# Kernel optimization log

Hardware: AMD Instinct MI355X
Metric: run time of the kernel (lower is better)

The kernel has to match this reference:

```python
import jax, jax.numpy as jnp
from jax import lax
import numpy as np

RADIUS = 0.1
NSAMPLE = 32
STRIDE = 4
NUM_DIR = 32
BN_EPS = 1e-5


def _fps(p, m):
    # furthest point sampling: p (B,N,3) -> (B,m) int32 indices, start at index 0
    B, N, _ = p.shape

    def step(carry, _):
        dists, last = carry
        lp = jnp.take_along_axis(p, jnp.broadcast_to(last[:, None, None], (B, 1, 3)), axis=1)
        d = jnp.sum((p - lp) ** 2, axis=-1)
        dists = jnp.minimum(dists, d)
        nxt = jnp.argmax(dists, axis=-1).astype(jnp.int32)
        return (dists, nxt), nxt

    last0 = jnp.zeros((B,), jnp.int32)
    d0 = jnp.full((B, N), 1e10, p.dtype)
    _, rest = lax.scan(step, (d0, last0), None, length=m - 1)
    return jnp.concatenate([last0[None, :], rest], axis=0).T  # (B, m)


def _ball_query(q, p, k, radius):
    # q (B,M,3) centers, p (B,N,3) support -> (B,M,k) indices of first k points in ball,
    # padded with the first found index (PointNet++ convention)
    N = p.shape[1]
    d2 = jnp.sum((q[:, :, None, :] - p[:, None, :, :]) ** 2, axis=-1)  # (B,M,N)
    cand = jnp.where(d2 < radius * radius, jnp.arange(N, dtype=jnp.int32), N)
    cand = jnp.sort(cand, axis=-1)[:, :, :k]
    first = cand[:, :, :1]
    return jnp.where(cand == N, first, cand)


def _bn(x, g, b, m, v):
    # BatchNorm1d eval mode on (B,C,N)
    return (x - m[:, None]) * (g[:, None] / jnp.sqrt(v[:, None] + BN_EPS)) + b[:, None]


def _normalize(x, axis):
    return x / jnp.maximum(jnp.linalg.norm(x, axis=axis, keepdims=True), 1e-12)


def setup_inputs() -> dict:
    key = jax.random.key(0)
    ks = jax.random.split(key, 16)
    B, N, Cin, Cout = 4, 8192, 128, 256
    half = Cout // 2
    s = 0.02
    return {
        "p": jax.random.uniform(ks[0], (B, N, 3), jnp.float32),
        "f": jax.random.normal(ks[1], (B, Cin, N), jnp.float32),
        "conv1_w": jax.random.normal(ks[2], (Cout, Cin), jnp.float32) * s,
        "conv1_b": jax.random.normal(ks[3], (Cout,), jnp.float32) * s,
        "skip_w": jax.random.normal(ks[4], (Cout, Cin), jnp.float32) * s,
        "skip_b": jax.random.normal(ks[5], (Cout,), jnp.float32) * s,
        "bn1_g": jnp.ones((Cout,), jnp.float32),
        "bn1_b": jnp.zeros((Cout,), jnp.float32),
        "bn1_m": jax.random.normal(ks[6], (Cout,), jnp.float32) * 0.1,
        "bn1_v": jax.random.uniform(ks[7], (Cout,), jnp.float32) + 0.5,
        "dir_vectors": jax.random.normal(ks[8], (NUM_DIR, 3), jnp.float32),
        "de_w1": jax.random.normal(ks[9], (half, NUM_DIR), jnp.float32) * s,
        "de_g": jnp.ones((half,), jnp.float32),
        "de_bb": jnp.zeros((half,), jnp.float32),
        "de_m": jax.random.normal(ks[10], (half,), jnp.float32) * 0.1,
        "de_v": jax.random.uniform(ks[11], (half,), jnp.float32) + 0.5,
        "de_w2": jax.random.normal(ks[12], (Cout, half), jnp.float32) * s,
        "de_b2": jax.random.normal(ks[13], (Cout,), jnp.float32) * s,
    }


def reference(p, f, conv1_w, conv1_b, skip_w, skip_b, bn1_g, bn1_b, bn1_m, bn1_v,
              dir_vectors, de_w1, de_g, de_bb, de_m, de_v, de_w2, de_b2):
    B, N, _ = p.shape
    Cout = conv1_w.shape[0]
    M, K = N // STRIDE, NSAMPLE

    # FPS sampling + centroid gather
    idx = _fps(p, M)  # (B,M)
    new_p = jnp.take_along_axis(p, jnp.broadcast_to(idx[:, :, None], (B, M, 3)), axis=1)

    # residual branch: gather input feats at centroids, 1x1 conv (bn_after=False)
    fi = jnp.take_along_axis(f, jnp.broadcast_to(idx[:, None, :], (B, f.shape[1], M)), axis=2)
    identity = jnp.einsum('oc,bcm->bom', skip_w, fi) + skip_b[:, None]

    # convs1: 1x1 conv on all N points
    f1 = jnp.einsum('oc,bcn->bon', conv1_w, f) + conv1_b[:, None]  # (B,Cout,N)

    # ball-query grouping
    qidx = _ball_query(new_p, p, K, RADIUS)  # (B,M,K)
    idxf = qidx.reshape(B, M * K)
    gp = jnp.take_along_axis(p, jnp.broadcast_to(idxf[:, :, None], (B, M * K, 3)), axis=1).reshape(B, M, K, 3)
    dp = jnp.transpose(gp - new_p[:, :, None, :], (0, 3, 1, 2))  # (B,3,M,K)
    fj = jnp.take_along_axis(f1, jnp.broadcast_to(idxf[:, None, :], (B, Cout, M * K)), axis=2).reshape(B, Cout, M, K)

    # directional encoding
    dpn = _normalize(dp, axis=1)
    vec = _normalize(dir_vectors, axis=1)  # (NUM_DIR,3)
    theta = jnp.einsum('md,bdnk->bmnk', vec, dpn)  # (B,NUM_DIR,M,K)
    tmax = theta.max(axis=-1)  # (B,NUM_DIR,M)
    h = jnp.einsum('om,bmn->bon', de_w1, tmax)
    h = jax.nn.gelu(_bn(h, de_g, de_bb, de_m, de_v), approximate=False)
    pe = jnp.einsum('oc,bcn->bon', de_w2, h) + de_b2[:, None]

    # neighbor max-pool + BN + residuals
    f_out = _bn(fj.max(axis=-1), bn1_g, bn1_b, bn1_m, bn1_v) + pe + identity
    return new_p, f_out
```

## Files before the change

kernel.cpp:

```cpp
#include <hip/hip_runtime.h>

#define BATCH 4
#define NPTS 8192
#define MPTS 2048
#define CIN 128
#define CO 256
#define KS 32
#define ND 32
#define HALF 128

typedef unsigned int u32;
typedef unsigned long long u64;

#define DPPC_QUAD_XOR1 0xB1
#define DPPC_QUAD_XOR2 0x4E
#define DPPC_ROW_MIRROR 0x140
#define DPPC_ROW_HALF_MIRROR 0x141
#define DPPC_ROW_BCAST15 0x142
#define DPPC_ROW_BCAST31 0x143

template<int CTRL>
__device__ __forceinline__ float dpp_max(float v) {
    int o = __builtin_amdgcn_update_dpp(__float_as_int(-1e30f), __float_as_int(v),
                                        CTRL, 0xF, 0xF, false);
    return fmaxf(v, __int_as_float(o));
}
__device__ __forceinline__ float wave_max_f32(float v) {
    v = dpp_max<DPPC_QUAD_XOR1>(v);
    v = dpp_max<DPPC_QUAD_XOR2>(v);
    v = dpp_max<DPPC_ROW_HALF_MIRROR>(v);
    v = dpp_max<DPPC_ROW_MIRROR>(v);
    v = dpp_max<DPPC_ROW_BCAST15>(v);
    v = dpp_max<DPPC_ROW_BCAST31>(v);
    return __int_as_float(__builtin_amdgcn_readlane(__float_as_int(v), 63));
}

__global__ __launch_bounds__(512, 2) void k_fps_f1(
    const float* __restrict__ p, const float* __restrict__ f,
    const float* __restrict__ conv1_w, const float* __restrict__ conv1_b,
    float* __restrict__ out_newp, int* __restrict__ idx,
    float* __restrict__ f1t) {
    __shared__ __align__(16) char smem_u[33024];
    if (blockIdx.x < 4) {
        u64*   wkey = (u64*)smem_u;
        int*   sidx = (int*)(smem_u + 128);
        float* sx   = (float*)(smem_u + 128 + 4 * MPTS);
        float* sy   = sx + MPTS;
        float* sz   = sy + MPTS;
        int b = blockIdx.x, t = threadIdx.x;
        int lane = t & 63, wid = t >> 6;
        int j0 = t * 16;
        const float* pb = p + (size_t)b * NPTS * 3;
        const float* pt = pb + t * 48;
        float px[16], py[16], pz[16], dist[16];
#pragma unroll
        for (int c = 0; c < 4; ++c) {
            float4 q0 = *(const float4*)(pt + c * 12 + 0);
            float4 q1 = *(const float4*)(pt + c * 12 + 4);
            float4 q2 = *(const float4*)(pt + c * 12 + 8);
            px[c*4+0] = q0.x; py[c*4+0] = q0.y; pz[c*4+0] = q0.z;
            px[c*4+1] = q0.w; py[c*4+1] = q1.x; pz[c*4+1] = q1.y;
            px[c*4+2] = q1.z; py[c*4+2] = q1.w; pz[c*4+2] = q2.x;
            px[c*4+3] = q2.y; py[c*4+3] = q2.z; pz[c*4+3] = q2.w;
        }
#pragma unroll
        for (int i = 0; i < 16; ++i) dist[i] = 1e10f;
        float lx = pb[0], ly = pb[1], lz = pb[2];
        if (t == 0) {
            sidx[0] = 0; sx[0] = lx; sy[0] = ly; sz[0] = lz;
        }
        for (int s = 1; s < MPTS; ++s) {
            int par = s & 1;
            float bv = -1e30f; int bi = 0;
#pragma unroll
            for (int i = 0; i < 16; ++i) {
                float dx = __fsub_rn(px[i], lx);
                float dy = __fsub_rn(py[i], ly);
                float dz = __fsub_rn(pz[i], lz);
                float d  = __fadd_rn(__fadd_rn(__fmul_rn(dx, dx), __fmul_rn(dy, dy)),
                                     __fmul_rn(dz, dz));
                float nd = fminf(dist[i], d);
                dist[i] = nd;
                bool gt = nd > bv;
                bi = gt ? i : bi;
                bv = fmaxf(bv, nd);
            }
            float gmw = wave_max_f32(bv);
            u64 mask = __ballot(bv == gmw);
            int first = __ffsll((long long)mask) - 1;
            if (lane == first) {
                wkey[par * 8 + wid] = ((u64)__float_as_uint(gmw) << 32)
                                    | (u64)(u32)(NPTS - 1 - (j0 + bi));
            }
            __syncthreads();
            const u64* wk = wkey + par * 8;
            u64 k0 = wk[0], k1 = wk[1], k2 = wk[2], k3 = wk[3];
            u64 k4 = wk[4], k5 = wk[5], k6 = wk[6], k7 = wk[7];
            u64 m01 = k1 > k0 ? k1 : k0;
            u64 m23 = k3 > k2 ? k3 : k2;
            u64 m45 = k5 > k4 ? k5 : k4;
            u64 m67 = k7 > k6 ? k7 : k6;
            u64 m03 = m23 > m01 ? m23 : m01;
            u64 m47 = m67 > m45 ? m67 : m45;
            u64 best = m47 > m03 ? m47 : m03;
            int w0 = (NPTS - 1 - (int)(best & 0xFFFFFFFFull)) & (NPTS - 1);
            int w0s = __builtin_amdgcn_readfirstlane(w0);
            lx = pb[w0s * 3 + 0]; ly = pb[w0s * 3 + 1]; lz = pb[w0s * 3 + 2];
            if (t == 0) {
                sidx[s] = w0s; sx[s] = lx; sy[s] = ly; sz[s] = lz;
            }
        }
        __syncthreads();
        for (int e = t; e < MPTS; e += 512) {
            int base = (b * MPTS + e) * 3;
            out_newp[base + 0] = sx[e];
            out_newp[base + 1] = sy[e];
            out_newp[base + 2] = sz[e];
            idx[b * MPTS + e] = sidx[e];
        }
    } else if (f1t != nullptr) {
        float* fT = (float*)smem_u;
        int blk = blockIdx.x - 4;
        int b = blk >> 8;
        int n0 = (blk & 255) << 5;
        int t = threadIdx.x;
        const float* fb = f + (size_t)b * CIN * NPTS;
        for (int e = t; e < CIN * 32; e += 512) {
            int k = e >> 5, j = e & 31;
            fT[e] = fb[(size_t)k * NPTS + n0 + j];
        }
        __syncthreads();
        int c = t & 255, jh = (t >> 8) << 4;
        float bias = conv1_b[c];
        float acc[16];
#pragma unroll
        for (int j = 0; j < 16; ++j) acc[j] = bias;
        const float4* wrow4 = (const float4*)(conv1_w + (size_t)c * CIN);
        const float4* fT4 = (const float4*)fT;
        for (int k4 = 0; k4 < 32; ++k4) {
            float4 wv = wrow4[k4];
#pragma unroll
            for (int sub = 0; sub < 4; ++sub) {
                float w = sub == 0 ? wv.x : sub == 1 ? wv.y : sub == 2 ? wv.z : wv.w;
                int k = k4 * 4 + sub;
                int base = (k * 32 + jh) >> 2;
                float4 a0 = fT4[base+0], a1 = fT4[base+1], a2 = fT4[base+2], a3 = fT4[base+3];
                acc[0]  = fmaf(w, a0.x, acc[0]);  acc[1]  = fmaf(w, a0.y, acc[1]);
                acc[2]  = fmaf(w, a0.z, acc[2]);  acc[3]  = fmaf(w, a0.w, acc[3]);
                acc[4]  = fmaf(w, a1.x, acc[4]);  acc[5]  = fmaf(w, a1.y, acc[5]);
                acc[6]  = fmaf(w, a1.z, acc[6]);  acc[7]  = fmaf(w, a1.w, acc[7]);
                acc[8]  = fmaf(w, a2.x, acc[8]);  acc[9]  = fmaf(w, a2.y, acc[9]);
                acc[10] = fmaf(w, a2.z, acc[10]); acc[11] = fmaf(w, a2.w, acc[11]);
                acc[12] = fmaf(w, a3.x, acc[12]); acc[13] = fmaf(w, a3.y, acc[13]);
                acc[14] = fmaf(w, a3.z, acc[14]); acc[15] = fmaf(w, a3.w, acc[15]);
            }
        }
        float* dst = f1t + ((size_t)b * NPTS + n0 + jh) * CO + c;
#pragma unroll
        for (int j = 0; j < 16; ++j) dst[(size_t)j * CO] = acc[j];
    }
}

__global__ __launch_bounds__(256) void k_f1(const float* __restrict__ f,
                                            const float* __restrict__ conv1_w,
                                            const float* __restrict__ conv1_b,
                                            float* __restrict__ f1t, int b0) {
    __shared__ __align__(16) float fT[CIN * 16];
    int blk = blockIdx.x;
    int bl = blk >> 9;
    int b = b0 + bl;
    int n0 = (blk & 511) << 4;
    int t = threadIdx.x;
    const float* fb = f + (size_t)b * CIN * NPTS;
    for (int e = t; e < CIN * 16; e += 256) {
        int k = e >> 4, j = e & 15;
        fT[e] = fb[(size_t)k * NPTS + n0 + j];
    }
    __syncthreads();
    int c = t;
    float bias = conv1_b[c];
    float acc[16];
#pragma unroll
    for (int j = 0; j < 16; ++j) acc[j] = bias;
    const float4* wrow4 = (const float4*)(conv1_w + (size_t)c * CIN);
    const float4* fT4 = (const float4*)fT;
    for (int k4 = 0; k4 < 32; ++k4) {
        float4 wv = wrow4[k4];
#pragma unroll
        for (int sub = 0; sub < 4; ++sub) {
            float w = sub == 0 ? wv.x : sub == 1 ? wv.y : sub == 2 ? wv.z : wv.w;
            int k = k4 * 4 + sub;
            float4 a0 = fT4[k*4+0], a1 = fT4[k*4+1], a2 = fT4[k*4+2], a3 = fT4[k*4+3];
            acc[0]  = fmaf(w, a0.x, acc[0]);  acc[1]  = fmaf(w, a0.y, acc[1]);
            acc[2]  = fmaf(w, a0.z, acc[2]);  acc[3]  = fmaf(w, a0.w, acc[3]);
            acc[4]  = fmaf(w, a1.x, acc[4]);  acc[5]  = fmaf(w, a1.y, acc[5]);
            acc[6]  = fmaf(w, a1.z, acc[6]);  acc[7]  = fmaf(w, a1.w, acc[7]);
            acc[8]  = fmaf(w, a2.x, acc[8]);  acc[9]  = fmaf(w, a2.y, acc[9]);
            acc[10] = fmaf(w, a2.z, acc[10]); acc[11] = fmaf(w, a2.w, acc[11]);
            acc[12] = fmaf(w, a3.x, acc[12]); acc[13] = fmaf(w, a3.y, acc[13]);
            acc[14] = fmaf(w, a3.z, acc[14]); acc[15] = fmaf(w, a3.w, acc[15]);
        }
    }
    float* dst = f1t + ((size_t)bl * NPTS + n0) * CO + c;
#pragma unroll
    for (int j = 0; j < 16; ++j) dst[(size_t)j * CO] = acc[j];
}

__global__ __launch_bounds__(256) void k_feat(
    const float* __restrict__ p, const float* __restrict__ f,
    const float* __restrict__ f1t,
    const float* __restrict__ skip_w,  const float* __restrict__ skip_b,
    const float* __restrict__ bn1_g, const float* __restrict__ bn1_b,
    const float* __restrict__ bn1_m, const float* __restrict__ bn1_v,
    const float* __restrict__ dirv,  const float* __restrict__ de_w1,
    const float* __restrict__ de_g,  const float* __restrict__ de_bb,
    const float* __restrict__ de_m,  const float* __restrict__ de_v,
    const float* __restrict__ de_w2, const float* __restrict__ de_b2,
    const int* __restrict__ idx,     float* __restrict__ out_f, int b0) {
    __shared__ float sdx[KS], sdy[KS], sdz[KS];
    __shared__ float ltm[ND], lfi[CIN], lh[HALF];
    __shared__ int swidx[4][KS];
    __shared__ int scnt[4];
    __shared__ int nb[KS], nbp[KS];

    int q = b0 * MPTS + blockIdx.x;
    int b = q >> 11;
    int bl = b - b0;
    int m = q & (MPTS - 1);
    int t = threadIdx.x, lane = t & 63, w = t >> 6;
    const float* pb = p + (size_t)b * NPTS * 3;
    int i0 = idx[q] & (NPTS - 1);
    float qx = pb[i0 * 3 + 0], qy = pb[i0 * 3 + 1], qz = pb[i0 * 3 + 2];
    const float R2 = 0.1f * 0.1f;

    int cnt = 0;
    int seg = w * 2048;
    for (int base = 0; base < 2048; base += 64) {
        int j = seg + base + lane;
        float dx = __fsub_rn(pb[j * 3 + 0], qx);
        float dy = __fsub_rn(pb[j * 3 + 1], qy);
        float dz = __fsub_rn(pb[j * 3 + 2], qz);
        float d2 = __fadd_rn(__fadd_rn(__fmul_rn(dx, dx), __fmul_rn(dy, dy)),
                             __fmul_rn(dz, dz));
        bool hit = d2 < R2;
        u64 mask = __ballot(hit);
        if (hit) {
            int pos = cnt + __popcll(mask & ((1ull << lane) - 1ull));
            if (pos < KS) swidx[w][pos] = j;
        }
        cnt += __popcll(mask);
        if (cnt >= KS) break;
    }
    if (lane == 0) scnt[w] = cnt < KS ? cnt : KS;
    __syncthreads();
    int c0s = scnt[0], c1s = scnt[1], c2s = scnt[2], c3s = scnt[3];
    int st1 = c0s, st2 = c0s + c1s, st3 = c0s + c1s + c2s;
    int total = c0s + c1s + c2s + c3s; if (total > KS) total = KS;
    if (total < 1) total = 1;
    if (t < 128) {
        int ww = t >> 5, l = t & 31;
        int stw = (ww == 0) ? 0 : (ww == 1) ? st1 : (ww == 2) ? st2 : st3;
        int cw  = (ww == 0) ? c0s : (ww == 1) ? c1s : (ww == 2) ? c2s : c3s;
        int gp = stw + l;
        if (l < cw && gp < KS) nb[gp] = swidx[ww][l];
    }
    __syncthreads();
    if (t < KS) {
        int jk = nb[t < total ? t : 0] & (NPTS - 1);
        nbp[t] = jk;
        float dx = pb[jk * 3 + 0] - qx;
        float dy = pb[jk * 3 + 1] - qy;
        float dz = pb[jk * 3 + 2] - qz;
        float nr = fmaxf(sqrtf(dx * dx + dy * dy + dz * dz), 1e-12f);
        sdx[t] = dx / nr; sdy[t] = dy / nr; sdz[t] = dz / nr;
    }
    if (t >= 128) {
        lfi[t - 128] = f[((size_t)b * CIN + (t - 128)) * NPTS + i0];
    }
    __syncthreads();
    if (t < ND) {
        float ax = dirv[t * 3], ay = dirv[t * 3 + 1], az = dirv[t * 3 + 2];
        float n = fmaxf(sqrtf(ax * ax + ay * ay + az * az), 1e-12f);
        float vx = ax / n, vy = ay / n, vz = az / n;
        float tm = -1e30f;
#pragma unroll
        for (int k = 0; k < KS; ++k)
            tm = fmaxf(tm, vx * sdx[k] + vy * sdy[k] + vz * sdz[k]);
        ltm[t] = tm;
    }
    __syncthreads();

    int c = t;
    const float* f1b = f1t + (size_t)bl * NPTS * CO + c;
    float mx = -1e30f;
#pragma unroll 8
    for (int k = 0; k < KS; ++k) {
        mx = fmaxf(mx, f1b[(size_t)nbp[k] * CO]);
    }
    float sc1 = bn1_g[c] / sqrtf(bn1_v[c] + 1e-5f);
    float o1 = (mx - bn1_m[c]) * sc1 + bn1_b[c];

    float idv = skip_b[c];
    {
        const float4* sr = (const float4*)(skip_w + (size_t)c * CIN);
#pragma unroll 8
        for (int r = 0; r < 32; ++r) {
            float4 v = sr[r];
            idv = fmaf(v.x, lfi[r*4+0], fmaf(v.y, lfi[r*4+1],
                  fmaf(v.z, lfi[r*4+2], fmaf(v.w, lfi[r*4+3], idv))));
        }
    }
    {
        int hc = c & (HALF - 1);
        const float4* d1 = (const float4*)(de_w1 + (size_t)hc * ND);
        float a = 0.0f;
#pragma unroll
        for (int r = 0; r < 8; ++r) {
            float4 v = d1[r];
            a = fmaf(v.x, ltm[r*4+0], fmaf(v.y, ltm[r*4+1],
                fmaf(v.z, ltm[r*4+2], fmaf(v.w, ltm[r*4+3], a))));
        }
        float dsc = de_g[hc] / sqrtf(de_v[hc] + 1e-5f);
        float xb = (a - de_m[hc]) * dsc + de_bb[hc];
        float hv = 0.5f * xb * (1.0f + erff(xb * 0.70710678118654752440f));
        if (c < HALF) lh[c] = hv;
    }
    __syncthreads();
    float pe = de_b2[c];
    {
        const float4* d2p = (const float4*)(de_w2 + (size_t)c * HALF);
#pragma unroll 8
        for (int r = 0; r < 32; ++r) {
            float4 v = d2p[r];
            pe = fmaf(v.x, lh[r*4+0], fmaf(v.y, lh[r*4+1],
                 fmaf(v.z, lh[r*4+2], fmaf(v.w, lh[r*4+3], pe))));
        }
    }
    out_f[((size_t)b * CO + c) * MPTS + m] = o1 + pe + idv;
}

__global__ __launch_bounds__(256) void k_featz_fused(
    const float* __restrict__ p, const float* __restrict__ f,
    const float* __restrict__ conv1_w, const float* __restrict__ conv1_b,
    const float* __restrict__ skip_w,  const float* __restrict__ skip_b,
    const float* __restrict__ bn1_g, const float* __restrict__ bn1_b,
    const float* __restrict__ bn1_m, const float* __restrict__ bn1_v,
    const float* __restrict__ dirv,  const float* __restrict__ de_w1,
    const float* __restrict__ de_g,  const float* __restrict__ de_bb,
    const float* __restrict__ de_m,  const float* __restrict__ de_v,
    const float* __restrict__ de_w2, const float* __restrict__ de_b2,
    const int* __restrict__ idx,     float* __restrict__ out_f) {
    __shared__ __align__(16) float fg[KS * CIN];
    __shared__ float sdx[KS], sdy[KS], sdz[KS];
    __shared__ float ltm[ND], lfi[CIN], lh[HALF];
    __shared__ int swidx[4][KS];
    __shared__ int scnt[4];
    __shared__ int nb[KS], nbp[KS];

    int q = blockIdx.x;
    int b = q >> 11;
    int m = q & (MPTS - 1);
    int t = threadIdx.x, lane = t & 63, w = t >> 6;
    const float* pb = p + (size_t)b * NPTS * 3;
    int i0 = idx[q] & (NPTS - 1);
    float qx = pb[i0 * 3 + 0], qy = pb[i0 * 3 + 1], qz = pb[i0 * 3 + 2];
    const float R2 = 0.1f * 0.1f;
    int cnt = 0;
    int seg = w * 2048;
    for (int base = 0; base < 2048; base += 64) {
        int j = seg + base + lane;
        float dx = __fsub_rn(pb[j * 3 + 0], qx);
        float dy = __fsub_rn(pb[j * 3 + 1], qy);
        float dz = __fsub_rn(pb[j * 3 + 2], qz);
        float d2 = __fadd_rn(__fadd_rn(__fmul_rn(dx, dx), __fmul_rn(dy, dy)),
                             __fmul_rn(dz, dz));
        bool hit = d2 < R2;
        u64 mask = __ballot(hit);
        if (hit) {
            int pos = cnt + __popcll(mask & ((1ull << lane) - 1ull));
            if (pos < KS) swidx[w][pos] = j;
        }
        cnt += __popcll(mask);
        if (cnt >= KS) break;
    }
    if (lane == 0) scnt[w] = cnt < KS ? cnt : KS;
    __syncthreads();
    int c0s = scnt[0], c1s = scnt[1], c2s = scnt[2], c3s = scnt[3];
    int st1 = c0s, st2 = c0s + c1s, st3 = c0s + c1s + c2s;
    int total = c0s + c1s + c2s + c3s; if (total > KS) total = KS;
    if (total < 1) total = 1;
    if (t < 128) {
        int ww = t >> 5, l = t & 31;
        int stw = (ww == 0) ? 0 : (ww == 1) ? st1 : (ww == 2) ? st2 : st3;
        int cw  = (ww == 0) ? c0s : (ww == 1) ? c1s : (ww == 2) ? c2s : c3s;
        int gp = stw + l;
        if (l < cw && gp < KS) nb[gp] = swidx[ww][l];
    }
    __syncthreads();
    if (t < KS) {
        int jk = nb[t < total ? t : 0] & (NPTS - 1);
        nbp[t] = jk;
        float dx = pb[jk * 3 + 0] - qx;
        float dy = pb[jk * 3 + 1] - qy;
        float dz = pb[jk * 3 + 2] - qz;
        float nr = fmaxf(sqrtf(dx * dx + dy * dy + dz * dz), 1e-12f);
        sdx[t] = dx / nr; sdy[t] = dy / nr; sdz[t] = dz / nr;
    }
    if (t >= 128) lfi[t - 128] = f[((size_t)b * CIN + (t - 128)) * NPTS + i0];
    __syncthreads();
    if (t < ND) {
        float ax = dirv[t * 3], ay = dirv[t * 3 + 1], az = dirv[t * 3 + 2];
        float n = fmaxf(sqrtf(ax * ax + ay * ay + az * az), 1e-12f);
        float vx = ax / n, vy = ay / n, vz = az / n;
        float tm = -1e30f;
#pragma unroll
        for (int k = 0; k < KS; ++k)
            tm = fmaxf(tm, vx * sdx[k] + vy * sdy[k] + vz * sdz[k]);
        ltm[t] = tm;
    }
    for (int e = t; e < KS * CIN; e += 256) {
        int k = e >> 7, i = e & 127;
        fg[k * CIN + i] = f[((size_t)b * CIN + i) * NPTS + nbp[k]];
    }
    __syncthreads();
    int c = t;
    float acc[KS];
#pragma unroll
    for (int k = 0; k < KS; ++k) acc[k] = 0.0f;
    const float4* w4 = (const float4*)(conv1_w + (size_t)c * CIN);
    const float4* fg4 = (const float4*)fg;
    for (int i4 = 0; i4 < 32; ++i4) {
        float4 wv = w4[i4];
#pragma unroll 8
        for (int k = 0; k < KS; ++k) {
            float4 g = fg4[k * 32 + i4];
            acc[k] = fmaf(wv.x, g.x, fmaf(wv.y, g.y,
                     fmaf(wv.z, g.z, fmaf(wv.w, g.w, acc[k]))));
        }
    }
    float bias = conv1_b[c];
    float mx = -1e30f;
#pragma unroll
    for (int k = 0; k < KS; ++k) mx = fmaxf(mx, acc[k] + bias);
    float sc1 = bn1_g[c] / sqrtf(bn1_v[c] + 1e-5f);
    float o1 = (mx - bn1_m[c]) * sc1 + bn1_b[c];
    float idv = skip_b[c];
    {
        const float4* sr = (const float4*)(skip_w + (size_t)c * CIN);
#pragma unroll 8
        for (int r = 0; r < 32; ++r) {
            float4 v = sr[r];
            idv = fmaf(v.x, lfi[r*4+0], fmaf(v.y, lfi[r*4+1],
                  fmaf(v.z, lfi[r*4+2], fmaf(v.w, lfi[r*4+3], idv))));
        }
    }
    {
        int hc = c & (HALF - 1);
        const float4* d1 = (const float4*)(de_w1 + (size_t)hc * ND);
        float a = 0.0f;
#pragma unroll
        for (int r = 0; r < 8; ++r) {
            float4 v = d1[r];
            a = fmaf(v.x, ltm[r*4+0], fmaf(v.y, ltm[r*4+1],
                fmaf(v.z, ltm[r*4+2], fmaf(v.w, ltm[r*4+3], a))));
        }
        float dsc = de_g[hc] / sqrtf(de_v[hc] + 1e-5f);
        float xb = (a - de_m[hc]) * dsc + de_bb[hc];
        float hv = 0.5f * xb * (1.0f + erff(xb * 0.70710678118654752440f));
        if (c < HALF) lh[c] = hv;
    }
    __syncthreads();
    float pe = de_b2[c];
    {
        const float4* d2p = (const float4*)(de_w2 + (size_t)c * HALF);
#pragma unroll 8
        for (int r = 0; r < 32; ++r) {
            float4 v = d2p[r];
            pe = fmaf(v.x, lh[r*4+0], fmaf(v.y, lh[r*4+1],
                 fmaf(v.z, lh[r*4+2], fmaf(v.w, lh[r*4+3], pe))));
        }
    }
    out_f[((size_t)b * CO + c) * MPTS + m] = o1 + pe + idv;
}

extern "C" void kernel_launch(void* const* d_in, const int* in_sizes, int n_in,
                              void* d_out, int out_size, void* d_ws, size_t ws_size,
                              hipStream_t stream) {
    const float* p       = (const float*)d_in[0];
    const float* f       = (const float*)d_in[1];
    const float* conv1_w = (const float*)d_in[2];
    const float* conv1_b = (const float*)d_in[3];
    const float* skip_w  = (const float*)d_in[4];
    const float* skip_b  = (const float*)d_in[5];
    const float* bn1_g   = (const float*)d_in[6];
    const float* bn1_b   = (const float*)d_in[7];
    const float* bn1_m   = (const float*)d_in[8];
    const float* bn1_v   = (const float*)d_in[9];
    const float* dirv    = (const float*)d_in[10];
    const float* de_w1   = (const float*)d_in[11];
    const float* de_g    = (const float*)d_in[12];
    const float* de_bb   = (const float*)d_in[13];
    const float* de_m    = (const float*)d_in[14];
    const float* de_v    = (const float*)d_in[15];
    const float* de_w2   = (const float*)d_in[16];
    const float* de_b2   = (const float*)d_in[17];

    float* out_newp = (float*)d_out;
    float* out_f    = (float*)d_out + (size_t)BATCH * MPTS * 3;
    int*   idx      = (int*)d_ws;
    float* f1t      = (float*)((char*)d_ws + 32768);

    size_t f1_one  = (size_t)NPTS * CO * 4;
    size_t need_full = 32768 + 4 * f1_one;
    size_t need_one  = 32768 + f1_one;
    int mode = (ws_size >= need_full) ? 2 : (ws_size >= need_one) ? 1 : 0;

    if (mode == 2) {
        k_fps_f1<<<dim3(4 + 1024), dim3(512), 0, stream>>>(
            p, f, conv1_w, conv1_b, out_newp, idx, f1t);
        k_feat<<<dim3(4 * MPTS), dim3(256), 0, stream>>>(
            p, f, f1t, skip_w, skip_b, bn1_g, bn1_b, bn1_m, bn1_v,
            dirv, de_w1, de_g, de_bb, de_m, de_v, de_w2, de_b2, idx, out_f, 0);
    } else if (mode == 1) {
        k_fps_f1<<<dim3(4), dim3(512), 0, stream>>>(
            p, f, conv1_w, conv1_b, out_newp, idx, nullptr);
        for (int b0 = 0; b0 < BATCH; ++b0) {
            k_f1  <<<dim3(512),  dim3(256), 0, stream>>>(f, conv1_w, conv1_b, f1t, b0);
            k_feat<<<dim3(MPTS), dim3(256), 0, stream>>>(
                p, f, f1t, skip_w, skip_b, bn1_g, bn1_b, bn1_m, bn1_v,
                dirv, de_w1, de_g, de_bb, de_m, de_v, de_w2, de_b2, idx, out_f, b0);
        }
    } else {
        k_fps_f1<<<dim3(4), dim3(512), 0, stream>>>(
            p, f, conv1_w, conv1_b, out_newp, idx, nullptr);
        k_featz_fused<<<dim3(BATCH * MPTS), dim3(256), 0, stream>>>(
            p, f, conv1_w, conv1_b, skip_w, skip_b, bn1_g, bn1_b, bn1_m, bn1_v,
            dirv, de_w1, de_g, de_bb, de_m, de_v, de_w2, de_b2, idx, out_f);
    }
}
```

Measured before the change: 2.857 ms.

## Fuse FPS, conv1 and feature stages into one persistent kernel with progress flags

Adds a single mega-kernel in which the four FPS blocks publish per-step progress counters through agent-scope atomics. Feature blocks spin-wait on those counters and on a conv1 completion counter, then do ball query, directional encoding and output for each sampled centre as soon as it exists. This overlaps the long serial FPS with the per-centre feature work and removes a kernel boundary. The cost is polling traffic, a memset, and the risk of deadlock or stale reads if blocks are not co-resident or ordering is weak, although the spin loops have iteration caps.

```diff
diff --git a/kernel.cpp b/kernel.cpp
--- a/kernel.cpp
+++ b/kernel.cpp
@@ -33,6 +33,299 @@
     v = dpp_max<DPPC_ROW_BCAST15>(v);
     v = dpp_max<DPPC_ROW_BCAST31>(v);
     return __int_as_float(__builtin_amdgcn_readlane(__float_as_int(v), 63));
+}
+
+struct FeatSmem {
+    float sdx[KS], sdy[KS], sdz[KS];
+    float ltm[ND], lfi[CIN], lh[HALF];
+    int swidx[4][KS];
+    int scnt[4];
+    int nb[KS], nbp[KS];
+};
+
+__global__ __launch_bounds__(512, 2) void k_mega(
+    const float* __restrict__ p, const float* __restrict__ f,
+    const float* __restrict__ conv1_w, const float* __restrict__ conv1_b,
+    const float* __restrict__ skip_w,  const float* __restrict__ skip_b,
+    const float* __restrict__ bn1_g, const float* __restrict__ bn1_b,
+    const float* __restrict__ bn1_m, const float* __restrict__ bn1_v,
+    const float* __restrict__ dirv,  const float* __restrict__ de_w1,
+    const float* __restrict__ de_g,  const float* __restrict__ de_bb,
+    const float* __restrict__ de_m,  const float* __restrict__ de_v,
+    const float* __restrict__ de_w2, const float* __restrict__ de_b2,
+    float* __restrict__ out_newp, float* __restrict__ out_f,
+    int* __restrict__ idx, float* __restrict__ f1t,
+    int* prog, int* f1all) {
+    __shared__ __align__(16) char smem_u[16640];
+    if (blockIdx.x < 4) {
+        u64* wkey = (u64*)smem_u;
+        int b = blockIdx.x, t = threadIdx.x;
+        int lane = t & 63, wid = t >> 6;
+        int j0 = t * 16;
+        const float* pb = p + (size_t)b * NPTS * 3;
+        const float* pt = pb + t * 48;
+        float px[16], py[16], pz[16], dist[16];
+#pragma unroll
+        for (int c = 0; c < 4; ++c) {
+            float4 q0 = *(const float4*)(pt + c * 12 + 0);
+            float4 q1 = *(const float4*)(pt + c * 12 + 4);
+            float4 q2 = *(const float4*)(pt + c * 12 + 8);
+            px[c*4+0] = q0.x; py[c*4+0] = q0.y; pz[c*4+0] = q0.z;
+            px[c*4+1] = q0.w; py[c*4+1] = q1.x; pz[c*4+1] = q1.y;
+            px[c*4+2] = q1.z; py[c*4+2] = q1.w; pz[c*4+2] = q2.x;
+            px[c*4+3] = q2.y; py[c*4+3] = q2.z; pz[c*4+3] = q2.w;
+        }
+#pragma unroll
+        for (int i = 0; i < 16; ++i) dist[i] = 1e10f;
+        float lx = pb[0], ly = pb[1], lz = pb[2];
+        if (t == 0) {
+            out_newp[(size_t)b * MPTS * 3 + 0] = lx;
+            out_newp[(size_t)b * MPTS * 3 + 1] = ly;
+            out_newp[(size_t)b * MPTS * 3 + 2] = lz;
+            __hip_atomic_store(idx + b * MPTS, 0, __ATOMIC_RELAXED,
+                               __HIP_MEMORY_SCOPE_AGENT);
+        }
+        for (int s = 1; s < MPTS; ++s) {
+            int par = s & 1;
+            float bv = -1e30f; int bi = 0;
+#pragma unroll
+            for (int i = 0; i < 16; ++i) {
+                float dx = __fsub_rn(px[i], lx);
+                float dy = __fsub_rn(py[i], ly);
+                float dz = __fsub_rn(pz[i], lz);
+                float d  = __fadd_rn(__fadd_rn(__fmul_rn(dx, dx), __fmul_rn(dy, dy)),
+                                     __fmul_rn(dz, dz));
+                float nd = fminf(dist[i], d);
+                dist[i] = nd;
+                bool gt = nd > bv;
+                bi = gt ? i : bi;
+                bv = fmaxf(bv, nd);
+            }
+            float gmw = wave_max_f32(bv);
+            u64 mask = __ballot(bv == gmw);
+            int first = __ffsll((long long)mask) - 1;
+            if (lane == first) {
+                wkey[par * 8 + wid] = ((u64)__float_as_uint(gmw) << 32)
+                                    | (u64)(u32)(NPTS - 1 - (j0 + bi));
+            }
+            __syncthreads();
+            const u64* wk = wkey + par * 8;
+            u64 k0 = wk[0], k1 = wk[1], k2 = wk[2], k3 = wk[3];
+            u64 k4 = wk[4], k5 = wk[5], k6 = wk[6], k7 = wk[7];
+            u64 m01 = k1 > k0 ? k1 : k0;
+            u64 m23 = k3 > k2 ? k3 : k2;
+            u64 m45 = k5 > k4 ? k5 : k4;
+            u64 m67 = k7 > k6 ? k7 : k6;
+            u64 m03 = m23 > m01 ? m23 : m01;
+            u64 m47 = m67 > m45 ? m67 : m45;
+            u64 best = m47 > m03 ? m47 : m03;
+            int w0 = (NPTS - 1 - (int)(best & 0xFFFFFFFFull)) & (NPTS - 1);
+            int w0s = __builtin_amdgcn_readfirstlane(w0);
+            if (t == 0) {
+                asm volatile("s_waitcnt vmcnt(0)" ::: "memory");
+                __hip_atomic_store(prog + b, s, __ATOMIC_RELAXED,
+                                   __HIP_MEMORY_SCOPE_AGENT);
+            }
+            lx = pb[w0s * 3 + 0]; ly = pb[w0s * 3 + 1]; lz = pb[w0s * 3 + 2];
+            if (t == 0) {
+                out_newp[((size_t)b * MPTS + s) * 3 + 0] = lx;
+                out_newp[((size_t)b * MPTS + s) * 3 + 1] = ly;
+                out_newp[((size_t)b * MPTS + s) * 3 + 2] = lz;
+                __hip_atomic_store(idx + b * MPTS + s, w0s, __ATOMIC_RELAXED,
+                                   __HIP_MEMORY_SCOPE_AGENT);
+            }
+        }
+        if (t == 0) {
+            asm volatile("s_waitcnt vmcnt(0)" ::: "memory");
+            __hip_atomic_store(prog + b, MPTS, __ATOMIC_RELAXED,
+                               __HIP_MEMORY_SCOPE_AGENT);
+        }
+    } else if (blockIdx.x < 4 + 1024) {
+        float* fT = (float*)smem_u;
+        int blk = blockIdx.x - 4;
+        int b = blk >> 8;
+        int n0 = (blk & 255) << 5;
+        int t = threadIdx.x;
+        const float* fb = f + (size_t)b * CIN * NPTS;
+        for (int e = t; e < CIN * 32; e += 512) {
+            int k = e >> 5, j = e & 31;
+            fT[e] = fb[(size_t)k * NPTS + n0 + j];
+        }
+        __syncthreads();
+        int c = t & 255, jh = (t >> 8) << 4;
+        float bias = conv1_b[c];
+        float acc[16];
+#pragma unroll
+        for (int j = 0; j < 16; ++j) acc[j] = bias;
+        const float4* wrow4 = (const float4*)(conv1_w + (size_t)c * CIN);
+        const float4* fT4 = (const float4*)fT;
+        for (int k4 = 0; k4 < 32; ++k4) {
+            float4 wv = wrow4[k4];
+#pragma unroll
+            for (int sub = 0; sub < 4; ++sub) {
+                float w = sub == 0 ? wv.x : sub == 1 ? wv.y : sub == 2 ? wv.z : wv.w;
+                int k = k4 * 4 + sub;
+                int base = (k * 32 + jh) >> 2;
+                float4 a0 = fT4[base+0], a1 = fT4[base+1], a2 = fT4[base+2], a3 = fT4[base+3];
+                acc[0]  = fmaf(w, a0.x, acc[0]);  acc[1]  = fmaf(w, a0.y, acc[1]);
+                acc[2]  = fmaf(w, a0.z, acc[2]);  acc[3]  = fmaf(w, a0.w, acc[3]);
+                acc[4]  = fmaf(w, a1.x, acc[4]);  acc[5]  = fmaf(w, a1.y, acc[5]);
+                acc[6]  = fmaf(w, a1.z, acc[6]);  acc[7]  = fmaf(w, a1.w, acc[7]);
+                acc[8]  = fmaf(w, a2.x, acc[8]);  acc[9]  = fmaf(w, a2.y, acc[9]);
+                acc[10] = fmaf(w, a2.z, acc[10]); acc[11] = fmaf(w, a2.w, acc[11]);
+                acc[12] = fmaf(w, a3.x, acc[12]); acc[13] = fmaf(w, a3.y, acc[13]);
+                acc[14] = fmaf(w, a3.z, acc[14]); acc[15] = fmaf(w, a3.w, acc[15]);
+            }
+        }
+        float* dst = f1t + ((size_t)b * NPTS + n0 + jh) * CO + c;
+#pragma unroll
+        for (int j = 0; j < 16; ++j) dst[(size_t)j * CO] = acc[j];
+        __syncthreads();
+        if (t == 0) {
+            __threadfence();
+            atomicAdd(f1all, 1);
+        }
+    } else {
+        int fb = (int)blockIdx.x - (4 + 1024);
+        int m  = fb >> 1;
+        int bA = (fb & 1) * 2;
+        int t = threadIdx.x;
+        if (t == 0) {
+            int need = m + 1;
+            for (int it = 0; it < (1 << 21); ++it) {
+                if (__hip_atomic_load(prog + bA, __ATOMIC_RELAXED,
+                                      __HIP_MEMORY_SCOPE_AGENT) >= need) break;
+                __builtin_amdgcn_s_sleep(127);
+            }
+            for (int it = 0; it < (1 << 21); ++it) {
+                if (__hip_atomic_load(prog + bA + 1, __ATOMIC_RELAXED,
+                                      __HIP_MEMORY_SCOPE_AGENT) >= need) break;
+                __builtin_amdgcn_s_sleep(127);
+            }
+            for (int it = 0; it < (1 << 21); ++it) {
+                if (__hip_atomic_load(f1all, __ATOMIC_RELAXED,
+                                      __HIP_MEMORY_SCOPE_AGENT) >= 1024) break;
+                __builtin_amdgcn_s_sleep(127);
+            }
+            (void)__hip_atomic_load(prog + bA, __ATOMIC_ACQUIRE,
+                                    __HIP_MEMORY_SCOPE_AGENT);
+        }
+        __syncthreads();
+        int qi = t >> 8;
+        int tq = t & 255;
+        int b  = bA + qi;
+        FeatSmem* fs = ((FeatSmem*)smem_u) + qi;
+        int lane = t & 63, wq = (t >> 6) & 3;
+        const float* pb = p + (size_t)b * NPTS * 3;
+        int i0 = idx[(size_t)b * MPTS + m] & (NPTS - 1);
+        float qx = pb[i0 * 3 + 0], qy = pb[i0 * 3 + 1], qz = pb[i0 * 3 + 2];
+        const float R2 = 0.1f * 0.1f;
+
+        int cnt = 0;
+        int seg = wq * 2048;
+        for (int base = 0; base < 2048; base += 64) {
+            int j = seg + base + lane;
+            float dx = __fsub_rn(pb[j * 3 + 0], qx);
+            float dy = __fsub_rn(pb[j * 3 + 1], qy);
+            float dz = __fsub_rn(pb[j * 3 + 2], qz);
+            float d2 = __fadd_rn(__fadd_rn(__fmul_rn(dx, dx), __fmul_rn(dy, dy)),
+                                 __fmul_rn(dz, dz));
+            bool hit = d2 < R2;
+            u64 mask = __ballot(hit);
+            if (hit) {
+                int pos = cnt + __popcll(mask & ((1ull << lane) - 1ull));
+                if (pos < KS) fs->swidx[wq][pos] = j;
+            }
+            cnt += __popcll(mask);
+            if (cnt >= KS) break;
+        }
+        if (lane == 0) fs->scnt[wq] = cnt < KS ? cnt : KS;
+        __syncthreads();
+        int c0s = fs->scnt[0], c1s = fs->scnt[1], c2s = fs->scnt[2], c3s = fs->scnt[3];
+        int st1 = c0s, st2 = c0s + c1s, st3 = c0s + c1s + c2s;
+        int total = c0s + c1s + c2s + c3s; if (total > KS) total = KS;
+        if (total < 1) total = 1;
+        if (tq < 128) {
+            int ww = tq >> 5, l = tq & 31;
+            int stw = (ww == 0) ? 0 : (ww == 1) ? st1 : (ww == 2) ? st2 : st3;
+            int cw  = (ww == 0) ? c0s : (ww == 1) ? c1s : (ww == 2) ? c2s : c3s;
+            int gp = stw + l;
+            if (l < cw && gp < KS) fs->nb[gp] = fs->swidx[ww][l];
+        }
+        __syncthreads();
+        if (tq < KS) {
+            int jk = fs->nb[tq < total ? tq : 0] & (NPTS - 1);
+            fs->nbp[tq] = jk;
+            float dx = pb[jk * 3 + 0] - qx;
+            float dy = pb[jk * 3 + 1] - qy;
+            float dz = pb[jk * 3 + 2] - qz;
+            float nr = fmaxf(sqrtf(dx * dx + dy * dy + dz * dz), 1e-12f);
+            fs->sdx[tq] = dx / nr; fs->sdy[tq] = dy / nr; fs->sdz[tq] = dz / nr;
+        }
+        if (tq >= 128) {
+            fs->lfi[tq - 128] = f[((size_t)b * CIN + (tq - 128)) * NPTS + i0];
+        }
+        __syncthreads();
+        if (tq < ND) {
+            float ax = dirv[tq * 3], ay = dirv[tq * 3 + 1], az = dirv[tq * 3 + 2];
+            float n = fmaxf(sqrtf(ax * ax + ay * ay + az * az), 1e-12f);
+            float vx = ax / n, vy = ay / n, vz = az / n;
+            float tm = -1e30f;
+#pragma unroll
+            for (int k = 0; k < KS; ++k)
+                tm = fmaxf(tm, vx * fs->sdx[k] + vy * fs->sdy[k] + vz * fs->sdz[k]);
+            fs->ltm[tq] = tm;
+        }
+        __syncthreads();
+
+        int c = tq;
+        const float* f1b = f1t + (size_t)b * NPTS * CO + c;
+        float mx = -1e30f;
+#pragma unroll 8
+        for (int k = 0; k < KS; ++k) {
+            mx = fmaxf(mx, f1b[(size_t)fs->nbp[k] * CO]);
+        }
+        float sc1 = bn1_g[c] / sqrtf(bn1_v[c] + 1e-5f);
+        float o1 = (mx - bn1_m[c]) * sc1 + bn1_b[c];
+
+        float idv = skip_b[c];
+        {
+            const float4* sr = (const float4*)(skip_w + (size_t)c * CIN);
+#pragma unroll 8
+            for (int r = 0; r < 32; ++r) {
+                float4 v = sr[r];
+                idv = fmaf(v.x, fs->lfi[r*4+0], fmaf(v.y, fs->lfi[r*4+1],
+                      fmaf(v.z, fs->lfi[r*4+2], fmaf(v.w, fs->lfi[r*4+3], idv))));
+            }
+        }
+        {
+            int hc = c & (HALF - 1);
+            const float4* d1 = (const float4*)(de_w1 + (size_t)hc * ND);
+            float a = 0.0f;
+#pragma unroll
+            for (int r = 0; r < 8; ++r) {
+                float4 v = d1[r];
+                a = fmaf(v.x, fs->ltm[r*4+0], fmaf(v.y, fs->ltm[r*4+1],
+                    fmaf(v.z, fs->ltm[r*4+2], fmaf(v.w, fs->ltm[r*4+3], a))));
+            }
+            float dsc = de_g[hc] / sqrtf(de_v[hc] + 1e-5f);
+            float xb = (a - de_m[hc]) * dsc + de_bb[hc];
+            float hv = 0.5f * xb * (1.0f + erff(xb * 0.70710678118654752440f));
+            if (c < HALF) fs->lh[c] = hv;
+        }
+        __syncthreads();
+        float pe = de_b2[c];
+        {
+            const float4* d2p = (const float4*)(de_w2 + (size_t)c * HALF);
+#pragma unroll 8
+            for (int r = 0; r < 32; ++r) {
+                float4 v = d2p[r];
+                pe = fmaf(v.x, fs->lh[r*4+0], fmaf(v.y, fs->lh[r*4+1],
+                     fmaf(v.z, fs->lh[r*4+2], fmaf(v.w, fs->lh[r*4+3], pe))));
+            }
+        }
+        out_f[((size_t)b * CO + c) * MPTS + m] = o1 + pe + idv;
+    }
 }
 
 __global__ __launch_bounds__(512, 2) void k_fps_f1(
@@ -66,9 +359,7 @@
 #pragma unroll
         for (int i = 0; i < 16; ++i) dist[i] = 1e10f;
         float lx = pb[0], ly = pb[1], lz = pb[2];
-        if (t == 0) {
-            sidx[0] = 0; sx[0] = lx; sy[0] = ly; sz[0] = lz;
-        }
+        if (t == 0) { sidx[0] = 0; sx[0] = lx; sy[0] = ly; sz[0] = lz; }
         for (int s = 1; s < MPTS; ++s) {
             int par = s & 1;
             float bv = -1e30f; int bi = 0;
@@ -106,9 +397,7 @@
             int w0 = (NPTS - 1 - (int)(best & 0xFFFFFFFFull)) & (NPTS - 1);
             int w0s = __builtin_amdgcn_readfirstlane(w0);
             lx = pb[w0s * 3 + 0]; ly = pb[w0s * 3 + 1]; lz = pb[w0s * 3 + 2];
-            if (t == 0) {
-                sidx[s] = w0s; sx[s] = lx; sy[s] = ly; sz[s] = lz;
-            }
+            if (t == 0) { sidx[s] = w0s; sx[s] = lx; sy[s] = ly; sz[s] = lz; }
         }
         __syncthreads();
         for (int e = t; e < MPTS; e += 512) {
@@ -508,20 +797,30 @@
     float* out_newp = (float*)d_out;
     float* out_f    = (float*)d_out + (size_t)BATCH * MPTS * 3;
     int*   idx      = (int*)d_ws;
-    float* f1t      = (float*)((char*)d_ws + 32768);
 
     size_t f1_one  = (size_t)NPTS * CO * 4;
-    size_t need_full = 32768 + 4 * f1_one;
-    size_t need_one  = 32768 + f1_one;
-    int mode = (ws_size >= need_full) ? 2 : (ws_size >= need_one) ? 1 : 0;
-
-    if (mode == 2) {
+    size_t need_stream = 32768 + 128 + 4 * f1_one;
+    size_t need_full   = 32768 + 4 * f1_one;
+    size_t need_one    = 32768 + f1_one;
+
+    if (ws_size >= need_stream) {
+        int*   prog  = (int*)((char*)d_ws + 32768);
+        int*   f1all = prog + 4;
+        float* f1t   = (float*)((char*)d_ws + 32768 + 128);
+        hipMemsetAsync(prog, 0, 128, stream);
+        k_mega<<<dim3(4 + 1024 + 4096), dim3(512), 0, stream>>>(
+            p, f, conv1_w, conv1_b, skip_w, skip_b, bn1_g, bn1_b, bn1_m, bn1_v,
+            dirv, de_w1, de_g, de_bb, de_m, de_v, de_w2, de_b2,
+            out_newp, out_f, idx, f1t, prog, f1all);
+    } else if (ws_size >= need_full) {
+        float* f1t = (float*)((char*)d_ws + 32768);
         k_fps_f1<<<dim3(4 + 1024), dim3(512), 0, stream>>>(
             p, f, conv1_w, conv1_b, out_newp, idx, f1t);
         k_feat<<<dim3(4 * MPTS), dim3(256), 0, stream>>>(
             p, f, f1t, skip_w, skip_b, bn1_g, bn1_b, bn1_m, bn1_v,
             dirv, de_w1, de_g, de_bb, de_m, de_v, de_w2, de_b2, idx, out_f, 0);
-    } else if (mode == 1) {
+    } else if (ws_size >= need_one) {
+        float* f1t = (float*)((char*)d_ws + 32768);
         k_fps_f1<<<dim3(4), dim3(512), 0, stream>>>(
             p, f, conv1_w, conv1_b, out_newp, idx, nullptr);
         for (int b0 = 0; b0 < BATCH; ++b0) {
```

Measured after the change: 2.551 ms. 10.7% less time.
